# Kernel optimization log

Hardware: AMD Instinct MI355X
Metric: run time of the kernel (lower is better)

The kernel has to match this reference:

```python
import jax, jax.numpy as jnp
import numpy as np

B, C, H, W = 8, 384, 32, 32
NH = 6
HD = C // NH          # 64
T = H * W             # 1024
EPS = 1e-5            # torch InstanceNorm2d default


def setup_inputs() -> dict:
    key = jax.random.key(0)
    ks = jax.random.split(key, 8)
    s = 1.0 / np.sqrt(C)  # keep pre-softmax logits in a sane range
    x = jax.random.normal(ks[0], (B, C, H, W), dtype=jnp.float32)
    Wq = jax.random.normal(ks[1], (C, C), dtype=jnp.float32) * s
    Wk = jax.random.normal(ks[2], (C, C), dtype=jnp.float32) * s
    Wv = jax.random.normal(ks[3], (C, C), dtype=jnp.float32) * s
    head_w = jax.random.normal(ks[4], (NH, NH), dtype=jnp.float32) * (1.0 / np.sqrt(NH))
    gamma = jnp.ones((NH,), dtype=jnp.float32)
    beta = jnp.zeros((NH,), dtype=jnp.float32)
    projW = jax.random.normal(ks[5], (C, C), dtype=jnp.float32) * s
    projb = jnp.zeros((C,), dtype=jnp.float32)
    return {"x": x, "Wq": Wq, "Wk": Wk, "Wv": Wv, "head_w": head_w,
            "gamma": gamma, "beta": beta, "projW": projW, "projb": projb}


def reference(x, Wq, Wk, Wv, head_w, gamma, beta, projW, projb):
    b, c, h, w = x.shape
    t = h * w
    scale = HD ** (-0.5)
    xf = x.reshape(b, c, t)                               # [B,C,T]
    # 1x1 convs == channel GEMMs; conv weight [Cout,Cin]
    q = jnp.einsum('oc,bct->bot', Wq, xf).reshape(b, NH, HD, t)
    k = jnp.einsum('oc,bct->bot', Wk, xf).reshape(b, NH, HD, t)
    v = jnp.einsum('oc,bct->bot', Wv, xf).reshape(b, NH, HD, t)
    # raw scores [B,h,T,T], scaled
    scores = jnp.einsum('bhdq,bhdt->bhqt', q, k) * scale
    # cross-head 1x1 conv mix: out-head g from in-head h
    mixed = jnp.einsum('gh,bhqt->bgqt', head_w, scores)
    attn = jax.nn.softmax(mixed, axis=-1)
    # InstanceNorm2d over spatial dims (q,T) per (b,head), biased variance
    mean = jnp.mean(attn, axis=(2, 3), keepdims=True)
    var = jnp.var(attn, axis=(2, 3), keepdims=True)
    attn = (attn - mean) * jax.lax.rsqrt(var + EPS)
    attn = attn * gamma[None, :, None, None] + beta[None, :, None, None]
    # value matmul: v is [B,h,d,T]
    out = jnp.einsum('bhqt,bhdt->bhqd', attn, v)          # [B,h,T,d]
    # faithful row-major reshape (matches torch .view(B, T, C))
    out = out.reshape(b, t, c)
    y = out @ projW.T + projb                              # Linear(C,C)
    return jnp.transpose(y, (0, 2, 1)).reshape(b, c, h, w)
```

## Files before the change

### kernel.cpp

```cpp
#include <hip/hip_runtime.h>
#include <hip/hip_bf16.h>
#include <cstdint>

typedef __bf16 bf16_t;
typedef __bf16 bf16x8 __attribute__((ext_vector_type(8)));
typedef float  f32x4  __attribute__((ext_vector_type(4)));
typedef int    i32x4  __attribute__((ext_vector_type(4)));

#define MFMA16(a, b, c) __builtin_amdgcn_mfma_f32_16x16x32_bf16((a), (b), (c), 0, 0, 0)

constexpr int BB = 8, CC = 384, NHH = 6, TT = 1024;

union U8 { uint4 u; bf16_t h[8]; };
union U2 { unsigned int u; bf16_t h[2]; };
union I4B { i32x4 i; bf16x8 v; };

static __device__ __forceinline__ void gload_lds16(const void* g, void* l) {
    __builtin_amdgcn_global_load_lds((const __attribute__((address_space(1))) void*)g,
                                     (__attribute__((address_space(3))) void*)l, 16, 0, 0);
}

__global__ __launch_bounds__(256) void castw_kernel(
    const float* __restrict__ w0, const float* __restrict__ w1,
    const float* __restrict__ w2, const float* __restrict__ w3,
    bf16_t* __restrict__ d0, bf16_t* __restrict__ d1,
    bf16_t* __restrict__ d2, bf16_t* __restrict__ d3)
{
    const int wi = blockIdx.y;
    const float* s = (wi == 0) ? w0 : (wi == 1) ? w1 : (wi == 2) ? w2 : w3;
    bf16_t*      d = (wi == 0) ? d0 : (wi == 1) ? d1 : (wi == 2) ? d2 : d3;
    const int idx = (blockIdx.x * 256 + threadIdx.x) * 8;
    f32x4 a = *(const f32x4*)(s + idx);
    f32x4 b = *(const f32x4*)(s + idx + 4);
    U8 o;
    #pragma unroll
    for (int j = 0; j < 4; ++j) { o.h[j] = (bf16_t)a[j]; o.h[4 + j] = (bf16_t)b[j]; }
    *(uint4*)(d + idx) = o.u;
}

__global__ __launch_bounds__(256) void qkv_kernel(
    const float* __restrict__ x,
    const bf16_t* __restrict__ Wq,
    const bf16_t* __restrict__ Wk,
    const bf16_t* __restrict__ Wv,
    bf16_t* __restrict__ qT,
    bf16_t* __restrict__ kT,
    bf16_t* __restrict__ vm,
    float*  __restrict__ vrs)
{
    const int tt = blockIdx.x;
    const int og = blockIdx.y;
    const int b  = blockIdx.z;
    const int t0 = tt * 64;
    const int tid  = threadIdx.x;
    const int lane = tid & 63;
    const int wid  = tid >> 6;
    const int quad = lane >> 4;
    const int l16  = lane & 15;

    __shared__ __align__(16) bf16_t xT[64][CC + 8];

    {
        const float* xb = x + (size_t)b * CC * TT;
        const int tq = tid & 7;
        const int cp = tid >> 3;
        #pragma unroll
        for (int pass = 0; pass < 6; ++pass) {
            const int c = (pass * 32 + cp) * 2;
            const float* r0 = xb + (size_t)c * TT + t0 + tq * 8;
            const float* r1 = r0 + TT;
            f32x4 a0 = *(const f32x4*)r0, a1 = *(const f32x4*)(r0 + 4);
            f32x4 b0 = *(const f32x4*)r1, b1 = *(const f32x4*)(r1 + 4);
            #pragma unroll
            for (int j = 0; j < 8; ++j) {
                U2 p;
                p.h[0] = (bf16_t)((j < 4) ? a0[j] : a1[j - 4]);
                p.h[1] = (bf16_t)((j < 4) ? b0[j] : b1[j - 4]);
                *(unsigned int*)&xT[tq * 8 + j][c] = p.u;
            }
        }
    }
    __syncthreads();

    const bf16_t* W = (og < 2) ? Wq : (og < 4) ? Wk : Wv;
    const int obase = (og & 1) * 192 + wid * 48;

    if (og < 4) {
        f32x4 acc[3][4];
        const f32x4 zero = {0.f, 0.f, 0.f, 0.f};
        #pragma unroll
        for (int mi = 0; mi < 3; ++mi)
            #pragma unroll
            for (int ni = 0; ni < 4; ++ni) acc[mi][ni] = zero;

        for (int k0 = 0; k0 < CC; k0 += 32) {
            bf16x8 afr[3];
            #pragma unroll
            for (int mi = 0; mi < 3; ++mi)
                afr[mi] = *(const bf16x8*)(W + (size_t)(obase + mi * 16 + l16) * CC + k0 + quad * 8);
            #pragma unroll
            for (int ni = 0; ni < 4; ++ni) {
                bf16x8 bfr = *(const bf16x8*)&xT[ni * 16 + l16][k0 + quad * 8];
                #pragma unroll
                for (int mi = 0; mi < 3; ++mi)
                    acc[mi][ni] = MFMA16(afr[mi], bfr, acc[mi][ni]);
            }
        }

        bf16_t* dst = (og < 2) ? qT : kT;
        #pragma unroll
        for (int mi = 0; mi < 3; ++mi)
            #pragma unroll
            for (int ni = 0; ni < 4; ++ni) {
                const int o0 = obase + mi * 16 + quad * 4;
                const int tl = t0 + ni * 16 + l16;
                U2 lo2, hi2;
                lo2.h[0] = (bf16_t)acc[mi][ni][0]; lo2.h[1] = (bf16_t)acc[mi][ni][1];
                hi2.h[0] = (bf16_t)acc[mi][ni][2]; hi2.h[1] = (bf16_t)acc[mi][ni][3];
                uint2 pk; pk.x = lo2.u; pk.y = hi2.u;
                *(uint2*)(dst + ((size_t)b * TT + tl) * CC + o0) = pk;
            }
    } else {
        f32x4 acc[4][3];
        const f32x4 zero = {0.f, 0.f, 0.f, 0.f};
        #pragma unroll
        for (int mi = 0; mi < 4; ++mi)
            #pragma unroll
            for (int ni = 0; ni < 3; ++ni) acc[mi][ni] = zero;

        for (int k0 = 0; k0 < CC; k0 += 32) {
            bf16x8 bfr[3];
            #pragma unroll
            for (int ni = 0; ni < 3; ++ni)
                bfr[ni] = *(const bf16x8*)(W + (size_t)(obase + ni * 16 + l16) * CC + k0 + quad * 8);
            #pragma unroll
            for (int mi = 0; mi < 4; ++mi) {
                bf16x8 afr = *(const bf16x8*)&xT[mi * 16 + l16][k0 + quad * 8];
                #pragma unroll
                for (int ni = 0; ni < 3; ++ni)
                    acc[mi][ni] = MFMA16(afr, bfr[ni], acc[mi][ni]);
            }
        }

        #pragma unroll
        for (int mi = 0; mi < 4; ++mi)
            #pragma unroll
            for (int ni = 0; ni < 3; ++ni) {
                const int ol  = obase + ni * 16 + l16;
                const int tl0 = mi * 16 + quad * 4;
                U2 lo2, hi2;
                lo2.h[0] = (bf16_t)acc[mi][ni][0]; lo2.h[1] = (bf16_t)acc[mi][ni][1];
                hi2.h[0] = (bf16_t)acc[mi][ni][2]; hi2.h[1] = (bf16_t)acc[mi][ni][3];
                uint2 pk; pk.x = lo2.u; pk.y = hi2.u;
                *(uint2*)(vm + ((size_t)b * CC + ol) * TT + t0 + tl0) = pk;
            }

        #pragma unroll
        for (int ni = 0; ni < 3; ++ni) {
            float s = 0.f;
            #pragma unroll
            for (int mi = 0; mi < 4; ++mi)
                #pragma unroll
                for (int r = 0; r < 4; ++r) s += acc[mi][ni][r];
            s += __shfl_xor(s, 16, 64);
            s += __shfl_xor(s, 32, 64);
            if (quad == 0)
                atomicAdd(&vrs[b * CC + obase + ni * 16 + l16], s);
        }
    }
}

__global__ __launch_bounds__(256, 1) void fused_attn(
    const bf16_t* __restrict__ qT,
    const bf16_t* __restrict__ kT,
    const bf16_t* __restrict__ vm,
    const float*  __restrict__ head_w,
    float* __restrict__ Up,
    float* __restrict__ lp,
    float* __restrict__ l2p)
{
    const int L  = blockIdx.x;
    const int b  = L & 7;
    const int rr = L >> 3;
    const int qt = rr & 15;
    const int tq = rr >> 4;
    const int T0 = tq * 256;
    const int stag = (rr & 1) * 4;

    const int tid = threadIdx.x, lane = tid & 63, wid = tid >> 6;
    const int quad = lane >> 4, l16 = lane & 15;

    __shared__ __align__(16) bf16_t sm[36864];
    const int  s3    = l16 & 7;
    const int  vswz  = (quad ^ ((l16 >> 1) & 3)) * 8;
    const int  addrA = ((quad & 1) * 32 + l16) * 4;
    const int  addrB = addrA + 64;
    const bool qlo   = (quad < 2);

    float mixc[36];
    #pragma unroll
    for (int j = 0; j < 36; ++j) {
        const float v = 0.125f * head_w[j];
        mixc[j] = __uint_as_float(__builtin_amdgcn_readfirstlane(__float_as_uint(v)));
    }

    bf16x8 qf[6][2];
    {
        const bf16_t* qp = qT + ((size_t)b * TT + qt * 64 + wid * 16 + l16) * CC + quad * 8;
        #pragma unroll
        for (int h = 0; h < 6; ++h)
            #pragma unroll
            for (int k2 = 0; k2 < 2; ++k2)
                qf[h][k2] = *(const bf16x8*)(qp + h * 64 + k2 * 32);
    }

    int koff[6], voff[6];
    #pragma unroll
    for (int i = 0; i < 6; ++i) {
        const int f = i * 256 + tid;
        const int krow = f / 48, kc = f - krow * 48;
        koff[i] = krow * CC + ((kc & 56) | ((kc ^ krow) & 7)) * 8;
        const int vrow = f >> 2, vc = f & 3;
        voff[i] = vrow * TT + ((vc ^ ((vrow >> 1) & 3)) * 8);
    }
    const bf16_t* kTb = kT + ((size_t)b * TT + T0) * CC;
    const bf16_t* vmb = vm + (size_t)b * CC * TT + T0;
    char* KsB = (char*)sm;
    char* VsB = (char*)sm + 49152;
    const int ldst = tid * 16;

    #pragma unroll
    for (int i = 0; i < 6; ++i)
        gload_lds16(kTb + (size_t)stag * 32 * CC + koff[i], KsB + i * 4096 + ldst);

    f32x4 U[6][4];
    const f32x4 zero = {0.f, 0.f, 0.f, 0.f};
    #pragma unroll
    for (int h = 0; h < 6; ++h)
        #pragma unroll
        for (int d = 0; d < 4; ++d) U[h][d] = zero;
    float lacc[6]  = {0.f, 0.f, 0.f, 0.f, 0.f, 0.f};
    float l2acc[6] = {0.f, 0.f, 0.f, 0.f, 0.f, 0.f};

    __syncthreads();

    for (int it = 0; it < 8; ++it) {
        const int lt = (it + stag) & 7;
        const int cb = it & 1;

        #pragma unroll
        for (int i = 0; i < 6; ++i)
            gload_lds16(vmb + lt * 32 + voff[i], VsB + i * 4096 + ldst);
        if (it < 7) {
            const int ltn = (lt + 1) & 7;
            #pragma unroll
            for (int i = 0; i < 6; ++i)
                gload_lds16(kTb + (size_t)ltn * 32 * CC + koff[i],
                            KsB + (cb ^ 1) * 24576 + i * 4096 + ldst);
        }

        const bf16_t* Kc = sm + cb * 12288;
        f32x4 S[6][2];
        __builtin_amdgcn_s_setprio(1);
        #pragma unroll
        for (int h = 0; h < 6; ++h) {
            #pragma unroll
            for (int blk = 0; blk < 2; ++blk) {
                const bf16_t* Ar = Kc + (size_t)(blk * 16 + l16) * CC + h * 64;
                bf16x8 a0 = *(const bf16x8*)(Ar + ((quad ^ s3) * 8));
                bf16x8 a1 = *(const bf16x8*)(Ar + (((4 + quad) ^ s3) * 8));
                f32x4 s = MFMA16(a0, qf[h][0], zero);
                S[h][blk] = MFMA16(a1, qf[h][1], s);
            }
        }
        __builtin_amdgcn_s_setprio(0);

        bf16x8 pa[6];
        #pragma unroll
        for (int g = 0; g < 6; ++g) {
            unsigned int uu[2][2];
            #pragma unroll
            for (int blk = 0; blk < 2; ++blk) {
                f32x4 m = mixc[g * 6] * S[0][blk];
                #pragma unroll
                for (int h2 = 1; h2 < 6; ++h2) m += mixc[g * 6 + h2] * S[h2][blk];
                f32x4 pv;
                #pragma unroll
                for (int r = 0; r < 4; ++r) pv[r] = __expf(fminf(m[r], 60.0f));
                lacc[g]  += pv[0] + pv[1] + pv[2] + pv[3];
                l2acc[g] += pv[0] * pv[0] + pv[1] * pv[1] + pv[2] * pv[2] + pv[3] * pv[3];
                U2 lo, hi;
                lo.h[0] = (bf16_t)pv[0]; lo.h[1] = (bf16_t)pv[1];
                hi.h[0] = (bf16_t)pv[2]; hi.h[1] = (bf16_t)pv[3];
                uu[blk][0] = lo.u; uu[blk][1] = hi.u;
            }
            int x0 = __builtin_amdgcn_ds_bpermute(addrA, (int)uu[0][0]);
            int y0 = __builtin_amdgcn_ds_bpermute(addrA, (int)uu[1][0]);
            int x1 = __builtin_amdgcn_ds_bpermute(addrA, (int)uu[0][1]);
            int y1 = __builtin_amdgcn_ds_bpermute(addrA, (int)uu[1][1]);
            int x2 = __builtin_amdgcn_ds_bpermute(addrB, (int)uu[0][0]);
            int y2 = __builtin_amdgcn_ds_bpermute(addrB, (int)uu[1][0]);
            int x3 = __builtin_amdgcn_ds_bpermute(addrB, (int)uu[0][1]);
            int y3 = __builtin_amdgcn_ds_bpermute(addrB, (int)uu[1][1]);
            I4B c;
            c.i = (i32x4){qlo ? x0 : y0, qlo ? x1 : y1, qlo ? x2 : y2, qlo ? x3 : y3};
            pa[g] = c.v;
        }

        __syncthreads();

        const bf16_t* Vb = sm + 24576;
        __builtin_amdgcn_s_setprio(1);
        #pragma unroll
        for (int h = 0; h < 6; ++h) {
            #pragma unroll
            for (int n2 = 0; n2 < 4; ++n2) {
                bf16x8 bv = *(const bf16x8*)(Vb + (size_t)(h * 64 + n2 * 16 + l16) * 32 + vswz);
                U[h][n2] = MFMA16(pa[h], bv, U[h][n2]);
            }
        }
        __builtin_amdgcn_s_setprio(0);

        __syncthreads();
    }

    #pragma unroll
    for (int g = 0; g < 6; ++g) {
        float l = lacc[g], l2 = l2acc[g];
        l  += __shfl_xor(l, 16, 64);  l  += __shfl_xor(l, 32, 64);
        l2 += __shfl_xor(l2, 16, 64); l2 += __shfl_xor(l2, 32, 64);
        if (quad == 0) {
            const size_t o = ((size_t)tq * 48 + b * 6 + g) * TT + qt * 64 + wid * 16 + l16;
            lp[o] = l; l2p[o] = l2;
        }
    }

    #pragma unroll
    for (int h = 0; h < 6; ++h) {
        float* Ub = Up + ((((size_t)tq * 8 + b) * 6 + h) * TT + qt * 64 + wid * 16) * 64;
        #pragma unroll
        for (int n2 = 0; n2 < 4; ++n2)
            #pragma unroll
            for (int r = 0; r < 4; ++r)
                Ub[(size_t)(quad * 4 + r) * 64 + n2 * 16 + l16] = U[h][n2][r];
    }
}

__global__ __launch_bounds__(256) void stats_kernel(
    const float* __restrict__ lp, const float* __restrict__ l2p,
    float* __restrict__ linv, float* __restrict__ sq)
{
    const int bg = blockIdx.x >> 2;
    const int q  = (blockIdx.x & 3) * 256 + threadIdx.x;
    const int tid = threadIdx.x;
    const float l  = lp [(size_t)bg * TT + q] + lp [(size_t)(48 + bg) * TT + q]
                   + lp [(size_t)(96 + bg) * TT + q] + lp [(size_t)(144 + bg) * TT + q];
    const float l2 = l2p[(size_t)bg * TT + q] + l2p[(size_t)(48 + bg) * TT + q]
                   + l2p[(size_t)(96 + bg) * TT + q] + l2p[(size_t)(144 + bg) * TT + q];
    const float inv = 1.0f / l;
    linv[bg * TT + q] = inv;
    float c = l2 * inv * inv;
    #pragma unroll
    for (int off = 1; off < 64; off <<= 1) c += __shfl_xor(c, off, 64);
    __shared__ float red[4];
    if ((tid & 63) == 0) red[tid >> 6] = c;
    __syncthreads();
    if (tid == 0) atomicAdd(&sq[bg], red[0] + red[1] + red[2] + red[3]);
}

__global__ __launch_bounds__(256) void proj_kernel(
    const float* __restrict__ Up,
    const float* __restrict__ linv,
    const float* __restrict__ vrs,
    const float* __restrict__ sumsq,
    const float* __restrict__ gamma,
    const float* __restrict__ beta,
    const bf16_t* __restrict__ projW,
    const float* __restrict__ projb,
    float* __restrict__ out)
{
    const int ts = blockIdx.x;
    const int b  = blockIdx.y;
    const int t0 = ts * 16;
    const int tid = threadIdx.x, lane = tid & 63, wid = tid >> 6;
    const int quad = lane >> 4, l16 = lane & 15;

    __shared__ float Ac[6], Cc[6], pb[CC];
    if (tid < 6) {
        const float ss  = sumsq[b * NHH + tid];
        const float var = fmaxf(ss - 1.0f, 0.0f) * (1.0f / 1048576.0f);
        const float a   = gamma[tid] * rsqrtf(var + 1e-5f);
        Ac[tid] = a;
        Cc[tid] = beta[tid] - a * (1.0f / 1024.0f);
    }
    for (int i = tid; i < CC; i += 256) pb[i] = projb[i];
    __syncthreads();

    f32x4 acc[6];
    const f32x4 zero = {0.f, 0.f, 0.f, 0.f};
    #pragma unroll
    for (int mi = 0; mi < 6; ++mi) acc[mi] = zero;

    constexpr size_t PST = (size_t)BB * NHH * TT * 64;
    const float* Ub = Up + (size_t)b * (NHH * TT * 64);
    for (int k0 = 0; k0 < CC; k0 += 32) {
        const int tl = t0 + l16;
        const int baseoff = tl * CC + k0 + quad * 8;
        const int hh = baseoff >> 16;
        const int d0 = baseoff & 63;
        const float li = linv[b * 6144 + (baseoff >> 6)];
        const float Al = Ac[hh] * li;
        const float Cb = Cc[hh];
        f32x4 u0 = *(const f32x4*)(Ub + baseoff)
                 + *(const f32x4*)(Ub + PST + baseoff)
                 + *(const f32x4*)(Ub + 2 * PST + baseoff)
                 + *(const f32x4*)(Ub + 3 * PST + baseoff);
        f32x4 u1 = *(const f32x4*)(Ub + baseoff + 4)
                 + *(const f32x4*)(Ub + PST + baseoff + 4)
                 + *(const f32x4*)(Ub + 2 * PST + baseoff + 4)
                 + *(const f32x4*)(Ub + 3 * PST + baseoff + 4);
        U8 z;
        #pragma unroll
        for (int j = 0; j < 8; ++j) {
            const float uv = (j < 4) ? u0[j] : u1[j - 4];
            z.h[j] = (bf16_t)(Al * uv + Cb * vrs[b * CC + hh * 64 + d0 + j]);
        }
        bf16x8 bfr = *(const bf16x8*)&z;
        #pragma unroll
        for (int mi = 0; mi < 6; ++mi) {
            const int o = wid * 96 + mi * 16 + l16;
            bf16x8 afr = *(const bf16x8*)(projW + (size_t)o * CC + k0 + quad * 8);
            acc[mi] = MFMA16(afr, bfr, acc[mi]);
        }
    }

    #pragma unroll
    for (int mi = 0; mi < 6; ++mi)
        #pragma unroll
        for (int r = 0; r < 4; ++r) {
            const int o  = wid * 96 + mi * 16 + quad * 4 + r;
            const int tl = t0 + l16;
            out[((size_t)b * CC + o) * TT + tl] = acc[mi][r] + pb[o];
        }
}

extern "C" void kernel_launch(void* const* d_in, const int* in_sizes, int n_in,
                              void* d_out, int out_size, void* d_ws, size_t ws_size,
                              hipStream_t stream)
{
    float* outp = (float*)d_out;
    char* ws = (char*)d_ws;

    size_t off = 0;
    auto alloc = [&](size_t bytes) {
        void* p = ws + off;
        off += (bytes + 255) & ~(size_t)255;
        return p;
    };

    const size_t szT = (size_t)BB * TT * CC * sizeof(bf16_t);
    const size_t szW = (size_t)CC * CC * sizeof(bf16_t);

    bf16_t* qTb = (bf16_t*)alloc(szT);
    bf16_t* kTb = (bf16_t*)alloc(szT);
    bf16_t* vmb = (bf16_t*)alloc(szT);
    bf16_t* Wqb = (bf16_t*)alloc(szW);
    bf16_t* Wkb = (bf16_t*)alloc(szW);
    bf16_t* Wvb = (bf16_t*)alloc(szW);
    bf16_t* PWb = (bf16_t*)alloc(szW);
    float*  Uh  = (float*)alloc((size_t)4 * BB * NHH * TT * 64 * sizeof(float));
    float*  lpb = (float*)alloc((size_t)4 * 48 * TT * sizeof(float));
    float*  l2b = (float*)alloc((size_t)4 * 48 * TT * sizeof(float));
    float*  lv  = (float*)alloc((size_t)48 * TT * sizeof(float));
    float*  vr  = (float*)alloc((size_t)BB * CC * sizeof(float));
    float*  sq  = (float*)alloc(48 * sizeof(float));

    hipMemsetAsync(vr, 0, (size_t)BB * CC * sizeof(float), stream);
    hipMemsetAsync(sq, 0, 48 * sizeof(float), stream);
    castw_kernel<<<dim3(72, 4), 256, 0, stream>>>(
        (const float*)d_in[1], (const float*)d_in[2], (const float*)d_in[3],
        (const float*)d_in[7], Wqb, Wkb, Wvb, PWb);
    qkv_kernel<<<dim3(16, 6, 8), 256, 0, stream>>>(
        (const float*)d_in[0], Wqb, Wkb, Wvb, qTb, kTb, vmb, vr);
    fused_attn<<<512, 256, 0, stream>>>(
        qTb, kTb, vmb, (const float*)d_in[4], Uh, lpb, l2b);
    stats_kernel<<<192, 256, 0, stream>>>(lpb, l2b, lv, sq);
    proj_kernel<<<dim3(64, 8), 256, 0, stream>>>(
        Uh, lv, vr, sq, (const float*)d_in[5], (const float*)d_in[6],
        PWb, (const float*)d_in[8], outp);
}
```

Before: 210.4 us.

## Halve QKV time tile, replace atomics with partial sums reduced in stats kernel

The QKV projection kernel now processes 32 tokens per block instead of 64, doubling grid size to 1536 blocks for better occupancy. The V row-sum atomics are replaced by per-tile partial writes, and the stats kernel (now one 1024-thread block per batch-head) reduces both the V partials and the sumsq without atomics. This removes the two memset launches. Proj loop gets unroll 2. Trade-off: weights are re-read from global twice as often in QKV, and stats runs only 48 blocks.

```diff
diff --git a/kernel.cpp b/kernel.cpp
--- a/kernel.cpp
+++ b/kernel.cpp
@@ -46,27 +46,27 @@
     bf16_t* __restrict__ qT,
     bf16_t* __restrict__ kT,
     bf16_t* __restrict__ vm,
-    float*  __restrict__ vrs)
+    float*  __restrict__ vrp)
 {
     const int tt = blockIdx.x;
     const int og = blockIdx.y;
     const int b  = blockIdx.z;
-    const int t0 = tt * 64;
+    const int t0 = tt * 32;
     const int tid  = threadIdx.x;
     const int lane = tid & 63;
     const int wid  = tid >> 6;
     const int quad = lane >> 4;
     const int l16  = lane & 15;
 
-    __shared__ __align__(16) bf16_t xT[64][CC + 8];
+    __shared__ __align__(16) bf16_t xT[32][CC + 8];
 
     {
         const float* xb = x + (size_t)b * CC * TT;
-        const int tq = tid & 7;
-        const int cp = tid >> 3;
-        #pragma unroll
-        for (int pass = 0; pass < 6; ++pass) {
-            const int c = (pass * 32 + cp) * 2;
+        const int tq = tid & 3;
+        const int cp = tid >> 2;
+        #pragma unroll
+        for (int pass = 0; pass < 3; ++pass) {
+            const int c = (pass * 64 + cp) * 2;
             const float* r0 = xb + (size_t)c * TT + t0 + tq * 8;
             const float* r1 = r0 + TT;
             f32x4 a0 = *(const f32x4*)r0, a1 = *(const f32x4*)(r0 + 4);
@@ -86,12 +86,12 @@
     const int obase = (og & 1) * 192 + wid * 48;
 
     if (og < 4) {
-        f32x4 acc[3][4];
+        f32x4 acc[3][2];
         const f32x4 zero = {0.f, 0.f, 0.f, 0.f};
         #pragma unroll
         for (int mi = 0; mi < 3; ++mi)
             #pragma unroll
-            for (int ni = 0; ni < 4; ++ni) acc[mi][ni] = zero;
+            for (int ni = 0; ni < 2; ++ni) acc[mi][ni] = zero;
 
         for (int k0 = 0; k0 < CC; k0 += 32) {
             bf16x8 afr[3];
@@ -99,7 +99,7 @@
             for (int mi = 0; mi < 3; ++mi)
                 afr[mi] = *(const bf16x8*)(W + (size_t)(obase + mi * 16 + l16) * CC + k0 + quad * 8);
             #pragma unroll
-            for (int ni = 0; ni < 4; ++ni) {
+            for (int ni = 0; ni < 2; ++ni) {
                 bf16x8 bfr = *(const bf16x8*)&xT[ni * 16 + l16][k0 + quad * 8];
                 #pragma unroll
                 for (int mi = 0; mi < 3; ++mi)
@@ -111,7 +111,7 @@
         #pragma unroll
         for (int mi = 0; mi < 3; ++mi)
             #pragma unroll
-            for (int ni = 0; ni < 4; ++ni) {
+            for (int ni = 0; ni < 2; ++ni) {
                 const int o0 = obase + mi * 16 + quad * 4;
                 const int tl = t0 + ni * 16 + l16;
                 U2 lo2, hi2;
@@ -121,10 +121,10 @@
                 *(uint2*)(dst + ((size_t)b * TT + tl) * CC + o0) = pk;
             }
     } else {
-        f32x4 acc[4][3];
+        f32x4 acc[2][3];
         const f32x4 zero = {0.f, 0.f, 0.f, 0.f};
         #pragma unroll
-        for (int mi = 0; mi < 4; ++mi)
+        for (int mi = 0; mi < 2; ++mi)
             #pragma unroll
             for (int ni = 0; ni < 3; ++ni) acc[mi][ni] = zero;
 
@@ -134,7 +134,7 @@
             for (int ni = 0; ni < 3; ++ni)
                 bfr[ni] = *(const bf16x8*)(W + (size_t)(obase + ni * 16 + l16) * CC + k0 + quad * 8);
             #pragma unroll
-            for (int mi = 0; mi < 4; ++mi) {
+            for (int mi = 0; mi < 2; ++mi) {
                 bf16x8 afr = *(const bf16x8*)&xT[mi * 16 + l16][k0 + quad * 8];
                 #pragma unroll
                 for (int ni = 0; ni < 3; ++ni)
@@ -143,7 +143,7 @@
         }
 
         #pragma unroll
-        for (int mi = 0; mi < 4; ++mi)
+        for (int mi = 0; mi < 2; ++mi)
             #pragma unroll
             for (int ni = 0; ni < 3; ++ni) {
                 const int ol  = obase + ni * 16 + l16;
@@ -159,13 +159,13 @@
         for (int ni = 0; ni < 3; ++ni) {
             float s = 0.f;
             #pragma unroll
-            for (int mi = 0; mi < 4; ++mi)
+            for (int mi = 0; mi < 2; ++mi)
                 #pragma unroll
                 for (int r = 0; r < 4; ++r) s += acc[mi][ni][r];
             s += __shfl_xor(s, 16, 64);
             s += __shfl_xor(s, 32, 64);
             if (quad == 0)
-                atomicAdd(&vrs[b * CC + obase + ni * 16 + l16], s);
+                vrp[((size_t)tt * 8 + b) * CC + obase + ni * 16 + l16] = s;
         }
     }
 }
@@ -346,13 +346,18 @@
     }
 }
 
-__global__ __launch_bounds__(256) void stats_kernel(
+__global__ __launch_bounds__(1024) void stats_kernel(
     const float* __restrict__ lp, const float* __restrict__ l2p,
-    float* __restrict__ linv, float* __restrict__ sq)
+    const float* __restrict__ vrp,
+    float* __restrict__ linv, float* __restrict__ sq, float* __restrict__ vr)
 {
-    const int bg = blockIdx.x >> 2;
-    const int q  = (blockIdx.x & 3) * 256 + threadIdx.x;
-    const int tid = threadIdx.x;
+    const int bg = blockIdx.x, tid = threadIdx.x;
+    const int b = bg / 6, g = bg - b * 6;
+
+    __shared__ float red[16];
+    __shared__ float vred[8][64];
+
+    const int q = tid;
     const float l  = lp [(size_t)bg * TT + q] + lp [(size_t)(48 + bg) * TT + q]
                    + lp [(size_t)(96 + bg) * TT + q] + lp [(size_t)(144 + bg) * TT + q];
     const float l2 = l2p[(size_t)bg * TT + q] + l2p[(size_t)(48 + bg) * TT + q]
@@ -362,10 +367,31 @@
     float c = l2 * inv * inv;
     #pragma unroll
     for (int off = 1; off < 64; off <<= 1) c += __shfl_xor(c, off, 64);
-    __shared__ float red[4];
     if ((tid & 63) == 0) red[tid >> 6] = c;
+
+    if (tid < 512) {
+        const int d = tid & 63, ck = tid >> 6;
+        float s = 0.f;
+        #pragma unroll
+        for (int t2 = 0; t2 < 4; ++t2) {
+            const int t = ck * 4 + t2;
+            s += vrp[((size_t)t * 8 + b) * CC + g * 64 + d];
+        }
+        vred[ck][d] = s;
+    }
     __syncthreads();
-    if (tid == 0) atomicAdd(&sq[bg], red[0] + red[1] + red[2] + red[3]);
+    if (tid == 0) {
+        float s = 0.f;
+        #pragma unroll
+        for (int k = 0; k < 16; ++k) s += red[k];
+        sq[bg] = s;
+    }
+    if (tid < 64) {
+        float s = 0.f;
+        #pragma unroll
+        for (int k = 0; k < 8; ++k) s += vred[k][tid];
+        vr[b * CC + g * 64 + tid] = s;
+    }
 }
 
 __global__ __launch_bounds__(256) void proj_kernel(
@@ -403,6 +429,7 @@
 
     constexpr size_t PST = (size_t)BB * NHH * TT * 64;
     const float* Ub = Up + (size_t)b * (NHH * TT * 64);
+    #pragma unroll 2
     for (int k0 = 0; k0 < CC; k0 += 32) {
         const int tl = t0 + l16;
         const int baseoff = tl * CC + k0 + quad * 8;
@@ -472,19 +499,18 @@
     float*  lpb = (float*)alloc((size_t)4 * 48 * TT * sizeof(float));
     float*  l2b = (float*)alloc((size_t)4 * 48 * TT * sizeof(float));
     float*  lv  = (float*)alloc((size_t)48 * TT * sizeof(float));
+    float*  vrp = (float*)alloc((size_t)32 * BB * CC * sizeof(float));
     float*  vr  = (float*)alloc((size_t)BB * CC * sizeof(float));
     float*  sq  = (float*)alloc(48 * sizeof(float));
 
-    hipMemsetAsync(vr, 0, (size_t)BB * CC * sizeof(float), stream);
-    hipMemsetAsync(sq, 0, 48 * sizeof(float), stream);
     castw_kernel<<<dim3(72, 4), 256, 0, stream>>>(
         (const float*)d_in[1], (const float*)d_in[2], (const float*)d_in[3],
         (const float*)d_in[7], Wqb, Wkb, Wvb, PWb);
-    qkv_kernel<<<dim3(16, 6, 8), 256, 0, stream>>>(
-        (const float*)d_in[0], Wqb, Wkb, Wvb, qTb, kTb, vmb, vr);
+    qkv_kernel<<<dim3(32, 6, 8), 256, 0, stream>>>(
+        (const float*)d_in[0], Wqb, Wkb, Wvb, qTb, kTb, vmb, vrp);
     fused_attn<<<512, 256, 0, stream>>>(
         qTb, kTb, vmb, (const float*)d_in[4], Uh, lpb, l2b);
-    stats_kernel<<<192, 256, 0, stream>>>(lpb, l2b, lv, sq);
+    stats_kernel<<<48, 1024, 0, stream>>>(lpb, l2b, vrp, lv, sq, vr);
     proj_kernel<<<dim3(64, 8), 256, 0, stream>>>(
         Uh, lv, vr, sq, (const float*)d_in[5], (const float*)d_in[6],
         PWb, (const float*)d_in[8], outp);
```

After: 219.0 us. 4.1% more time.
